# Kernel optimization log

Hardware: AMD Instinct MI355X
Metric: run time of the kernel (lower is better)

## Reference

```python
import jax, jax.numpy as jnp
import numpy as np

B, L, D = 8, 2048, 2048
NH, HD = 32, 64          # num_heads, head_dim (D = NH*HD)
CS = 16                  # inner_net_chunk_size
BASE_LR = 1.0            # inner-loop base learning rate
EPS = 1e-6
ROPE_BASE = 10000.0


def setup_inputs() -> dict:
    key = jax.random.key(0)
    ks = jax.random.split(key, 6)
    s = 0.02
    return {
        "hidden_states": jax.random.normal(ks[0], (B, L, D), jnp.float32),
        "wq": jax.random.normal(ks[1], (D, D), jnp.float32) * s,
        "wk": jax.random.normal(ks[2], (D, D), jnp.float32) * s,
        "wv": jax.random.normal(ks[3], (D, D), jnp.float32) * s,
        "wo": jax.random.normal(ks[4], (D, D), jnp.float32) * s,
        "W1": jax.random.normal(ks[5], (NH, HD, HD), jnp.float32) * s,
        "b1": jnp.zeros((NH, 1, HD), jnp.float32),
        "ttt_norm_weight": jnp.ones((NH, HD), jnp.float32),
        "ttt_norm_bias": jnp.zeros((NH, HD), jnp.float32),
    }


def _rotate_half(x):
    x1, x2 = jnp.split(x, 2, axis=-1)
    return jnp.concatenate((-x2, x1), axis=-1)


def _permute_qk(x):
    b, h, l, f = x.shape
    return x.reshape(b, h, l, f // 2, 2).transpose(0, 1, 2, 4, 3).reshape(b, h, l, f)


def _undo_permute_qk(x):
    b, h, l, f = x.shape
    return x.reshape(b, h, l, 2, f // 2).transpose(0, 1, 2, 4, 3).reshape(b, h, l, f)


def _ln_fwd(x, g, b):
    mu = x.mean(-1, keepdims=True)
    var = ((x - mu) ** 2).mean(-1, keepdims=True)
    xh = (x - mu) * jax.lax.rsqrt(var + EPS)
    return g * xh + b


def _ln_fused_l2_bwd(x, target, g, b):
    # grad of 0.5*||LN(x) - target||^2 w.r.t. x, fused (TTT inner-loop loss grad)
    f = x.shape[-1]
    mu = x.mean(-1, keepdims=True)
    var = ((x - mu) ** 2).mean(-1, keepdims=True)
    std = jnp.sqrt(var + EPS)
    xh = (x - mu) / std
    gout = (g * xh + b) - target
    gxh = gout * g
    return (f * gxh - gxh.sum(-1, keepdims=True)
            - xh * (gxh * xh).sum(-1, keepdims=True)) / (f * std)


def reference(hidden_states, wq, wk, wv, wo, W1, b1, ttt_norm_weight, ttt_norm_bias):
    Bx, Lx, Dx = hidden_states.shape
    nc = Lx // CS

    def proj(w):  # [B,L,D] -> [B,NH,L,HD]
        return (hidden_states @ w).reshape(Bx, Lx, NH, HD).transpose(0, 2, 1, 3)

    XQ, XK, XV = proj(wq), proj(wk), proj(wv)

    # rotary embedding (with permute/undo as in the source)
    inv_freq = 1.0 / (ROPE_BASE ** (jnp.arange(0, HD, 2, dtype=jnp.float32) / HD))
    freqs = jnp.outer(jnp.arange(Lx, dtype=jnp.float32), inv_freq)
    emb = jnp.concatenate((freqs, freqs), axis=-1)
    cos, sin = jnp.cos(emb)[None, None], jnp.sin(emb)[None, None]
    XQ, XK = _permute_qk(XQ), _permute_qk(XK)
    XQ = XQ * cos + _rotate_half(XQ) * sin
    XK = XK * cos + _rotate_half(XK) * sin
    XQ, XK = _undo_permute_qk(XQ), _undo_permute_qk(XK)

    def chunk(x):  # [B,NH,L,HD] -> [nc,B,NH,CS,HD]
        return x.reshape(Bx, NH, nc, CS, HD).transpose(2, 0, 1, 3, 4)

    XQc, XKc, XVc = chunk(XQ), chunk(XK), chunk(XV)

    g = ttt_norm_weight[None, :, None, :]   # [1,NH,1,HD]
    bb = ttt_norm_bias[None, :, None, :]

    token_idx = 1.0 / jnp.arange(1, CS + 1, dtype=jnp.float32)   # buffer from __init__
    eta = BASE_LR * token_idx                                    # [CS]
    tril_eta = jnp.tril(jnp.ones((CS, CS), jnp.float32)) * eta[:, None]
    last_eta = eta[-1]

    W1_0 = jnp.broadcast_to(W1[None], (Bx, NH, HD, HD))
    b1_0 = jnp.broadcast_to(b1[None], (Bx, NH, 1, HD))

    def step(carry, xs):
        W1s, b1s = carry
        xq, xk, xv = xs                                          # [B,NH,CS,HD]
        Z1 = jnp.einsum('bhkf,bhfg->bhkg', xk, W1s) + b1s
        grad = _ln_fused_l2_bwd(Z1, xv - xk, g, bb)              # dl/dZ1
        attn = jnp.tril(jnp.einsum('bhkf,bhlf->bhkl', xq, xk))   # causal within chunk
        b1_bar = b1s - jnp.einsum('kl,bhlf->bhkf', tril_eta, grad)
        Z1_bar = (jnp.einsum('bhkf,bhfg->bhkg', xq, W1s)
                  - jnp.einsum('bhkl,bhlf->bhkf', eta[None, None, :, None] * attn, grad)
                  + b1_bar)
        W1_new = W1s - last_eta * jnp.einsum('bhkf,bhkg->bhfg', xk, grad)
        b1_new = b1s - last_eta * grad.sum(-2, keepdims=True)
        out = xq + _ln_fwd(Z1_bar, g, bb)                        # residual + post-LN
        return (W1_new, b1_new), out

    _, outs = jax.lax.scan(step, (W1_0, b1_0), (XQc, XKc, XVc))  # [nc,B,NH,CS,HD]
    out = (outs.transpose(1, 2, 0, 3, 4).reshape(Bx, NH, Lx, HD)
               .transpose(0, 2, 1, 3).reshape(Bx, Lx, Dx))
    return out @ wo
```

## Files before the change

kernel.cpp:

```cpp
#include <hip/hip_runtime.h>

typedef __bf16 bf16;
typedef __bf16 bf16x4 __attribute__((ext_vector_type(4)));
typedef __bf16 bf16x8 __attribute__((ext_vector_type(8)));
typedef float floatx4 __attribute__((ext_vector_type(4)));

#define BB 8
#define LL 2048
#define DD 2048
#define NHH 32
#define HDD 64

#define MFMA16(a, b, c) __builtin_amdgcn_mfma_f32_16x16x32_bf16(a, b, c, 0, 0, 0)

__device__ __forceinline__ void gl_lds16(const void* g, void* l) {
  __builtin_amdgcn_global_load_lds((const __attribute__((address_space(1))) void*)g,
                                   (__attribute__((address_space(3))) void*)l, 16, 0, 0);
}

__global__ __launch_bounds__(256) void cast_bf16(const float* __restrict__ src,
                                                 bf16* __restrict__ dst)
{
  size_t i = ((size_t)blockIdx.x * 256 + threadIdx.x) * 8;
  floatx4 a = *(const floatx4*)(src + i);
  floatx4 b = *(const floatx4*)(src + i + 4);
  bf16x8 v;
  v[0] = (bf16)a[0]; v[1] = (bf16)a[1]; v[2] = (bf16)a[2]; v[3] = (bf16)a[3];
  v[4] = (bf16)b[0]; v[5] = (bf16)b[1]; v[6] = (bf16)b[2]; v[7] = (bf16)b[3];
  *(bf16x8*)(dst + i) = v;
}

__global__ __launch_bounds__(256) void transpose1(const float* __restrict__ src,
                                                  bf16* __restrict__ dst)
{
  __shared__ float tile[64][65];
  const int t = threadIdx.x;
  const int col = t & 63, rw = t >> 6;
  const int bx = blockIdx.x * 64, by = blockIdx.y * 64;
  for (int i = rw; i < 64; i += 4)
    tile[i][col] = src[(size_t)(by + i) * DD + bx + col];
  __syncthreads();
  for (int i = rw; i < 64; i += 4)
    dst[(size_t)(bx + i) * DD + by + col] = (bf16)tile[col][i];
}

template<int AIDX, int EPI, int RP>
__global__ __launch_bounds__(256) void gemm_bt(const bf16* __restrict__ Ab,
    const bf16* __restrict__ BT, void* __restrict__ Cv)
{
  constexpr int Kd = 2048;
  __shared__ alignas(16) bf16 As[128 * 64];
  __shared__ alignas(16) bf16 Bs[128 * 64];
  const int t = threadIdx.x;
  const int id = blockIdx.y * 16 + blockIdx.x;
  const int swz = (id & 7) * 256 + (id >> 3);
  const int bn = swz & 15, bm = swz >> 4;
  const int wave = t >> 6, lane = t & 63;
  const int m16 = lane & 15, quad = lane >> 4;
  floatx4 acc[2][8] = {};
  const int r0 = t >> 3;
  const int scc = (t & 7) ^ (r0 & 7);
  const bf16* Bb = BT + (size_t)(bn * 128) * Kd;
  char* AsB = (char*)As + wave * 1024;
  char* BsB = (char*)Bs + wave * 1024;

  for (int k0 = 0; k0 < Kd; k0 += 64) {
    for (int i = 0; i < 4; ++i) {
      int r = r0 + 32 * i;
      int col = k0 + scc * 8;
      const bf16* ga;
      if (AIDX == 0) {
        ga = Ab + (size_t)(bm * 128 + r) * Kd + col;
      } else {
        int R = bm * 128 + r;
        int b = R >> 11, l = R & 2047;
        int h = col >> 6, f = col & 63;
        ga = Ab + (((size_t)(b * NHH + h) * LL + l) * HDD + f);
      }
      gl_lds16(ga, AsB + i * 4096);
      gl_lds16(Bb + (size_t)r * Kd + col, BsB + i * 4096);
    }
    __syncthreads();
    const int sw = m16 & 7;
    for (int kk = 0; kk < 2; ++kk) {
      bf16x8 af[2], bfr[8];
      const int c = ((kk * 4 + quad) ^ sw) * 8;
      for (int mt = 0; mt < 2; ++mt)
        af[mt] = *(const bf16x8*)&As[(wave * 32 + mt * 16 + m16) * 64 + c];
      for (int nt = 0; nt < 8; ++nt)
        bfr[nt] = *(const bf16x8*)&Bs[(nt * 16 + m16) * 64 + c];
      for (int mt = 0; mt < 2; ++mt)
        for (int nt = 0; nt < 8; ++nt)
          acc[mt][nt] = MFMA16(af[mt], bfr[nt], acc[mt][nt]);
    }
    __syncthreads();
  }

  float invf[8];
  if (RP) {
#pragma unroll
    for (int nt = 0; nt < 8; ++nt) {
      int col = bn * 128 + nt * 16 + m16;
      int i = (col >> 1) & 31;
      invf[nt] = __expf(-(float)i * 0.28782313662425573f);
    }
  }

  for (int mt = 0; mt < 2; ++mt)
    for (int nt = 0; nt < 8; ++nt)
      for (int rg = 0; rg < 4; ++rg) {
        int row = bm * 128 + wave * 32 + mt * 16 + quad * 4 + rg;
        int col = bn * 128 + nt * 16 + m16;
        float v = acc[mt][nt][rg];
        if (RP) {
          float o = __shfl_xor(v, 1, 64);
          float sn, cs;
          __sincosf((float)(row & 2047) * invf[nt], &sn, &cs);
          v = (m16 & 1) ? (v * cs + o * sn) : (v * cs - o * sn);
        }
        if (EPI == 0) {
          ((float*)Cv)[(size_t)row * DD + col] = v;
        } else {
          int b = row >> 11, l = row & 2047;
          int h = col >> 6, f = col & 63;
          ((bf16*)Cv)[((size_t)(b * NHH + h) * LL + l) * HDD + f] = (bf16)v;
        }
      }
}

__global__ __launch_bounds__(256) void ttt_scan(
    const bf16* Q, const bf16* __restrict__ Kx,
    const bf16* __restrict__ V, const float* __restrict__ W1g,
    const float* __restrict__ b1g, const float* __restrict__ gw,
    const float* __restrict__ gb, bf16* O)
{
  const int bh = blockIdx.x, h = bh & 31;
  const int t = threadIdx.x;
  const int wave = t >> 6, lane = t & 63;
  const int q = lane >> 4, i16 = lane & 15;
  const int kr = t >> 4, sr = t & 15, f0 = sr * 4;

  __shared__ alignas(16) bf16 W1Th[64 * 72];
  __shared__ alignas(16) bf16 W1Tl[64 * 72];
  __shared__ alignas(16) bf16 xkTs[64 * 24];
  __shared__ alignas(16) bf16 gTh[64 * 24];
  __shared__ alignas(16) bf16 gTl[64 * 24];
  __shared__ alignas(16) bf16 Pm[16 * 24];
  __shared__ alignas(16) float Z1s[2][16 * 68];

  floatx4 accW[4];
  const float* Wg = W1g + (size_t)h * 4096;
  for (int mt = 0; mt < 4; ++mt)
    for (int r = 0; r < 4; ++r)
      accW[mt][r] = Wg[(16 * mt + 4 * q + r) * 64 + 16 * wave + i16];
  float b1r = b1g[h * 64 + 16 * wave + i16];

  for (int mt = 0; mt < 4; ++mt) {
    bf16x4 h4, l4;
    for (int r = 0; r < 4; ++r) {
      float w = accW[mt][r];
      bf16 hi = (bf16)w;
      h4[r] = hi; l4[r] = (bf16)(w - (float)hi);
    }
    int base = (16 * wave + i16) * 72 + 16 * mt + 4 * q;
    *(bf16x4*)&W1Th[base] = h4;
    *(bf16x4*)&W1Tl[base] = l4;
  }

  float gq[4], bq[4];
  for (int j = 0; j < 4; ++j) {
    gq[j] = gw[h * 64 + f0 + j];
    bq[j] = gb[h * 64 + f0 + j];
  }
  float etar[4];
  for (int r = 0; r < 4; ++r) etar[r] = 1.0f / (float)(4 * q + r + 1);

  const size_t qbase = (size_t)bh * (LL * HDD);
  const int foff = i16 * 64 + q * 8;
  const int poff = kr * 64 + f0;

  bf16x8 ak0 = *(const bf16x8*)(Kx + qbase + foff);
  bf16x8 ak1 = *(const bf16x8*)(Kx + qbase + foff + 32);
  bf16x8 aq0 = *(const bf16x8*)(Q  + qbase + foff);
  bf16x8 aq1 = *(const bf16x8*)(Q  + qbase + foff + 32);
  bf16x4 rq = *(const bf16x4*)(Q  + qbase + poff);
  bf16x4 rk = *(const bf16x4*)(Kx + qbase + poff);
  bf16x4 rv = *(const bf16x4*)(V  + qbase + poff);

  __syncthreads();

  for (int c = 0; c < 128; ++c) {
    const int pb = c & 1;
    for (int j = 0; j < 4; ++j)
      xkTs[(f0 + j) * 24 + kr] = (bf16)((float)rk[j] * -0.0625f);

    bf16x8 whi[2], wlo[2];
    {
      int wb = (16 * wave + i16) * 72 + q * 8;
      whi[0] = *(const bf16x8*)&W1Th[wb];
      whi[1] = *(const bf16x8*)&W1Th[wb + 32];
      wlo[0] = *(const bf16x8*)&W1Tl[wb];
      wlo[1] = *(const bf16x8*)&W1Tl[wb + 32];
    }
    {
      floatx4 z = {b1r, b1r, b1r, b1r};
      z = MFMA16(ak0, whi[0], z);
      z = MFMA16(ak1, whi[1], z);
      z = MFMA16(ak0, wlo[0], z);
      z = MFMA16(ak1, wlo[1], z);
      for (int r = 0; r < 4; ++r)
        Z1s[pb][(4 * q + r) * 68 + 16 * wave + i16] = z[r];
    }
    if (wave == 0) {
      floatx4 at = {};
      at = MFMA16(aq0, ak0, at);
      at = MFMA16(aq1, ak1, at);
      for (int r = 0; r < 4; ++r) {
        int krow = 4 * q + r;
        float pv = (i16 <= krow) ? -(at[r] + 1.0f) * etar[r] : 0.0f;
        Pm[krow * 24 + i16] = (bf16)pv;
      }
    }
    __syncthreads();

    {
      floatx4 z4 = *(const floatx4*)&Z1s[pb][kr * 68 + f0];
      float tg[4], sum = 0.f, ssq = 0.f;
      for (int j = 0; j < 4; ++j) {
        tg[j] = (float)rv[j] - (float)rk[j];
        sum += z4[j]; ssq += z4[j] * z4[j];
      }
      for (int m = 1; m < 16; m <<= 1) { sum += __shfl_xor(sum, m, 64); ssq += __shfl_xor(ssq, m, 64); }
      float mu = sum * (1.f / 64.f);
      float var = ssq * (1.f / 64.f) - mu * mu;
      float rstd = rsqrtf(var + 1e-6f);
      float xh[4], gx[4], s1 = 0.f, s2 = 0.f;
      for (int j = 0; j < 4; ++j) {
        xh[j] = (z4[j] - mu) * rstd;
        float go = gq[j] * xh[j] + bq[j] - tg[j];
        gx[j] = go * gq[j];
        s1 += gx[j]; s2 += gx[j] * xh[j];
      }
      for (int m = 1; m < 16; m <<= 1) { s1 += __shfl_xor(s1, m, 64); s2 += __shfl_xor(s2, m, 64); }
      for (int j = 0; j < 4; ++j) {
        float gr = (64.f * gx[j] - s1 - xh[j] * s2) * (rstd * (1.f / 64.f));
        bf16 hi = (bf16)gr;
        gTh[(f0 + j) * 24 + kr] = hi;
        gTl[(f0 + j) * 24 + kr] = (bf16)(gr - (float)hi);
      }
    }
    __syncthreads();

    const size_t nb = qbase + (size_t)(c + 1) * 1024;
    bf16x8 nak0 = *(const bf16x8*)(Kx + nb + foff);
    bf16x8 nak1 = *(const bf16x8*)(Kx + nb + foff + 32);
    bf16x8 naq0 = *(const bf16x8*)(Q  + nb + foff);
    bf16x8 naq1 = *(const bf16x8*)(Q  + nb + foff + 32);
    bf16x4 nrq = *(const bf16x4*)(Q  + nb + poff);
    bf16x4 nrk = *(const bf16x4*)(Kx + nb + poff);
    bf16x4 nrv = *(const bf16x4*)(V  + nb + poff);

    {
      bf16x8 pf  = *(const bf16x8*)&Pm[i16 * 24 + (q & 1) * 8];
      const bf16* gT = (q < 2) ? gTh : gTl;
      bf16x8 bgp = *(const bf16x8*)&gT[(16 * wave + i16) * 24 + (q & 1) * 8];
      floatx4 zb = {b1r, b1r, b1r, b1r};
      zb = MFMA16(aq0, whi[0], zb);
      zb = MFMA16(aq1, whi[1], zb);
      zb = MFMA16(aq0, wlo[0], zb);
      zb = MFMA16(aq1, wlo[1], zb);
      zb = MFMA16(pf, bgp, zb);
      for (int r = 0; r < 4; ++r)
        Z1s[pb][(4 * q + r) * 68 + 16 * wave + i16] = zb[r];

      for (int mt = 0; mt < 4; ++mt) {
        bf16x8 axk = *(const bf16x8*)&xkTs[(16 * mt + i16) * 24 + (q & 1) * 8];
        accW[mt] = MFMA16(axk, bgp, accW[mt]);
      }
      for (int mt = 0; mt < 4; ++mt) {
        bf16x4 h4, l4;
        for (int r = 0; r < 4; ++r) {
          float w = accW[mt][r];
          bf16 hi = (bf16)w;
          h4[r] = hi; l4[r] = (bf16)(w - (float)hi);
        }
        int base = (16 * wave + i16) * 72 + 16 * mt + 4 * q;
        *(bf16x4*)&W1Th[base] = h4;
        *(bf16x4*)&W1Tl[base] = l4;
      }
      {
        const bf16* rh = &gTh[(16 * wave + i16) * 24];
        const bf16* rl = &gTl[(16 * wave + i16) * 24];
        bf16x8 a0 = *(const bf16x8*)rh, a1 = *(const bf16x8*)(rh + 8);
        bf16x8 a2 = *(const bf16x8*)rl, a3 = *(const bf16x8*)(rl + 8);
        float s = 0.f;
        for (int j = 0; j < 8; ++j)
          s += (float)a0[j] + (float)a1[j] + (float)a2[j] + (float)a3[j];
        b1r -= 0.0625f * s;
      }
    }
    __syncthreads();

    {
      floatx4 z4 = *(const floatx4*)&Z1s[pb][kr * 68 + f0];
      float sum = 0.f, ssq = 0.f;
      for (int j = 0; j < 4; ++j) { sum += z4[j]; ssq += z4[j] * z4[j]; }
      for (int m = 1; m < 16; m <<= 1) { sum += __shfl_xor(sum, m, 64); ssq += __shfl_xor(ssq, m, 64); }
      float mu = sum * (1.f / 64.f);
      float var = ssq * (1.f / 64.f) - mu * mu;
      float rstd = rsqrtf(var + 1e-6f);
      bf16x4 o4;
      for (int j = 0; j < 4; ++j)
        o4[j] = (bf16)((float)rq[j] + gq[j] * ((z4[j] - mu) * rstd) + bq[j]);
      *(bf16x4*)(O + qbase + (size_t)c * 1024 + poff) = o4;
    }
    ak0 = nak0; ak1 = nak1; aq0 = naq0; aq1 = naq1;
    rq = nrq; rk = nrk; rv = nrv;
  }
}

extern "C" void kernel_launch(void* const* d_in, const int* in_sizes, int n_in,
                              void* d_out, int out_size, void* d_ws, size_t ws_size,
                              hipStream_t stream)
{
  const float* X  = (const float*)d_in[0];
  const float* wq = (const float*)d_in[1];
  const float* wk = (const float*)d_in[2];
  const float* wv = (const float*)d_in[3];
  const float* wo = (const float*)d_in[4];
  const float* W1 = (const float*)d_in[5];
  const float* b1 = (const float*)d_in[6];
  const float* gw = (const float*)d_in[7];
  const float* gb = (const float*)d_in[8];

  bf16* ws = (bf16*)d_ws;
  const size_t NEl = (size_t)BB * LL * DD;
  bf16* Qb = ws;
  bf16* Kb = ws + NEl;
  bf16* WT = ws + 2 * NEl;
  bf16* Vb = (bf16*)d_out;
  bf16* Xb = (bf16*)d_out + NEl;

  cast_bf16<<<dim3(16384), 256, 0, stream>>>(X, Xb);
  transpose1<<<dim3(32, 32), 256, 0, stream>>>(wq, WT);
  gemm_bt<0, 1, 1><<<dim3(16, 128), 256, 0, stream>>>(Xb, WT, Qb);
  transpose1<<<dim3(32, 32), 256, 0, stream>>>(wk, WT);
  gemm_bt<0, 1, 1><<<dim3(16, 128), 256, 0, stream>>>(Xb, WT, Kb);
  transpose1<<<dim3(32, 32), 256, 0, stream>>>(wv, WT);
  gemm_bt<0, 1, 0><<<dim3(16, 128), 256, 0, stream>>>(Xb, WT, Vb);
  ttt_scan<<<dim3(256), 256, 0, stream>>>(Qb, Kb, Vb, W1, b1, gw, gb, Qb);
  transpose1<<<dim3(32, 32), 256, 0, stream>>>(wo, WT);
  gemm_bt<1, 0, 0><<<dim3(16, 128), 256, 0, stream>>>(Qb, WT, d_out);
}
```

Measured before the change: 1.202 ms.

## Fuse Q, K, V projections into one GEMM sharing the X tile

Replaces three separate projection GEMMs with a single 512-thread kernel that loads each X tile once and multiplies it against all three transposed weight tiles, applying rotary embedding in the epilogue for Q and K. All three weight transposes now live in separate buffers so they can be used together. A fallback path converts fp32 X to bf16 on the fly inside the GEMM when the workspace is too small. This cuts X reads to a third and removes launches, but it raises register pressure with 24 accumulator tiles per wave and uses more shared memory per block.

```diff
diff --git a/kernel.cpp b/kernel.cpp
--- a/kernel.cpp
+++ b/kernel.cpp
@@ -42,6 +42,115 @@
   __syncthreads();
   for (int i = rw; i < 64; i += 4)
     dst[(size_t)(bx + i) * DD + by + col] = (bf16)tile[col][i];
+}
+
+template<int AFP>
+__global__ __launch_bounds__(512) void gemm_qkv(const void* __restrict__ Xv,
+    const bf16* __restrict__ BTq, const bf16* __restrict__ BTk,
+    const bf16* __restrict__ BTv,
+    bf16* __restrict__ Qo, bf16* __restrict__ Ko, bf16* __restrict__ Vo)
+{
+  constexpr int Kd = 2048;
+  __shared__ alignas(16) bf16 As[128 * 64];
+  __shared__ alignas(16) bf16 Bs[3][128 * 64];
+  const int t = threadIdx.x;
+  const int id = blockIdx.y * 16 + blockIdx.x;
+  const int swz = (id & 7) * 256 + (id >> 3);
+  const int bn = swz & 15, bm = swz >> 4;
+  const int wv = t >> 6, lane = t & 63;
+  const int q = lane >> 4, i16 = lane & 15;
+  const int wm = wv >> 2, wn = wv & 3;
+  const int srow = lane >> 3, scol = lane & 7;
+
+  floatx4 acc[3][4][2] = {};
+  char* AsB = (char*)As + wv * 2048;
+  const bf16* Bg[3] = {BTq, BTk, BTv};
+
+  for (int k0 = 0; k0 < Kd; k0 += 64) {
+#pragma unroll
+    for (int i = 0; i < 2; ++i) {
+      int r = (wv * 2 + i) * 8 + srow;
+      int cc = scol ^ (r & 7);
+      if (AFP == 0) {
+        gl_lds16((const bf16*)Xv + (size_t)(bm * 128 + r) * Kd + k0 + cc * 8,
+                 AsB + i * 1024);
+      } else {
+        const float* src = (const float*)Xv + (size_t)(bm * 128 + r) * Kd + k0 + cc * 8;
+        floatx4 f0 = *(const floatx4*)src;
+        floatx4 f1 = *(const floatx4*)(src + 4);
+        bf16x8 v;
+        v[0] = (bf16)f0[0]; v[1] = (bf16)f0[1]; v[2] = (bf16)f0[2]; v[3] = (bf16)f0[3];
+        v[4] = (bf16)f1[0]; v[5] = (bf16)f1[1]; v[6] = (bf16)f1[2]; v[7] = (bf16)f1[3];
+        *(bf16x8*)((char*)As + (wv * 2 + i) * 1024 + lane * 16) = v;
+      }
+    }
+#pragma unroll
+    for (int w = 0; w < 3; ++w)
+#pragma unroll
+      for (int i = 0; i < 2; ++i) {
+        int r = (wv * 2 + i) * 8 + srow;
+        int cc = scol ^ (r & 7);
+        gl_lds16(Bg[w] + (size_t)(bn * 128 + r) * Kd + k0 + cc * 8,
+                 (char*)Bs[w] + wv * 2048 + i * 1024);
+      }
+    __syncthreads();
+
+#pragma unroll
+    for (int kk = 0; kk < 2; ++kk) {
+      bf16x8 af[4];
+#pragma unroll
+      for (int mt = 0; mt < 4; ++mt) {
+        int r = wm * 64 + mt * 16 + i16;
+        af[mt] = *(const bf16x8*)&As[r * 64 + ((kk * 4 + q) ^ (r & 7)) * 8];
+      }
+#pragma unroll
+      for (int w = 0; w < 3; ++w) {
+        bf16x8 bfr[2];
+#pragma unroll
+        for (int nt = 0; nt < 2; ++nt) {
+          int r = wn * 32 + nt * 16 + i16;
+          bfr[nt] = *(const bf16x8*)&Bs[w][r * 64 + ((kk * 4 + q) ^ (r & 7)) * 8];
+        }
+#pragma unroll
+        for (int mt = 0; mt < 4; ++mt)
+#pragma unroll
+          for (int nt = 0; nt < 2; ++nt)
+            acc[w][mt][nt] = MFMA16(af[mt], bfr[nt], acc[w][mt][nt]);
+      }
+    }
+    __syncthreads();
+  }
+
+  float invf[2];
+#pragma unroll
+  for (int nt = 0; nt < 2; ++nt) {
+    int col = bn * 128 + wn * 32 + nt * 16 + i16;
+    int i = (col >> 1) & 31;
+    invf[nt] = __expf(-(float)i * 0.28782313662425573f);
+  }
+#pragma unroll
+  for (int w = 0; w < 3; ++w) {
+    bf16* Co = (w == 0) ? Qo : (w == 1) ? Ko : Vo;
+#pragma unroll
+    for (int mt = 0; mt < 4; ++mt)
+#pragma unroll
+      for (int nt = 0; nt < 2; ++nt)
+#pragma unroll
+        for (int rg = 0; rg < 4; ++rg) {
+          int row = bm * 128 + wm * 64 + mt * 16 + q * 4 + rg;
+          int col = bn * 128 + wn * 32 + nt * 16 + i16;
+          float v = acc[w][mt][nt][rg];
+          if (w < 2) {
+            float o = __shfl_xor(v, 1, 64);
+            float sn, cs;
+            __sincosf((float)(row & 2047) * invf[nt], &sn, &cs);
+            v = (i16 & 1) ? (v * cs + o * sn) : (v * cs - o * sn);
+          }
+          int b = row >> 11, l = row & 2047;
+          int h = col >> 6, f = col & 63;
+          Co[((size_t)(b * NHH + h) * LL + l) * HDD + f] = (bf16)v;
+        }
+  }
 }
 
 template<int AIDX, int EPI, int RP>
@@ -335,20 +444,36 @@
 
   bf16* ws = (bf16*)d_ws;
   const size_t NEl = (size_t)BB * LL * DD;
+  const size_t WEl = (size_t)DD * DD;
   bf16* Qb = ws;
   bf16* Kb = ws + NEl;
-  bf16* WT = ws + 2 * NEl;
   bf16* Vb = (bf16*)d_out;
-  bf16* Xb = (bf16*)d_out + NEl;
-
-  cast_bf16<<<dim3(16384), 256, 0, stream>>>(X, Xb);
-  transpose1<<<dim3(32, 32), 256, 0, stream>>>(wq, WT);
-  gemm_bt<0, 1, 1><<<dim3(16, 128), 256, 0, stream>>>(Xb, WT, Qb);
-  transpose1<<<dim3(32, 32), 256, 0, stream>>>(wk, WT);
-  gemm_bt<0, 1, 1><<<dim3(16, 128), 256, 0, stream>>>(Xb, WT, Kb);
-  transpose1<<<dim3(32, 32), 256, 0, stream>>>(wv, WT);
-  gemm_bt<0, 1, 0><<<dim3(16, 128), 256, 0, stream>>>(Xb, WT, Vb);
-  ttt_scan<<<dim3(256), 256, 0, stream>>>(Qb, Kb, Vb, W1, b1, gw, gb, Qb);
-  transpose1<<<dim3(32, 32), 256, 0, stream>>>(wo, WT);
-  gemm_bt<1, 0, 0><<<dim3(16, 128), 256, 0, stream>>>(Qb, WT, d_out);
-}
+
+  const size_t need = (2 * NEl + 3 * WEl) * sizeof(bf16);
+  if (ws_size >= need) {
+    bf16* BTq = ws + 2 * NEl;
+    bf16* BTk = BTq + WEl;
+    bf16* BTv = BTk + WEl;
+    bf16* Xb  = (bf16*)d_out + NEl;
+    cast_bf16<<<dim3(16384), 256, 0, stream>>>(X, Xb);
+    transpose1<<<dim3(32, 32), 256, 0, stream>>>(wq, BTq);
+    transpose1<<<dim3(32, 32), 256, 0, stream>>>(wk, BTk);
+    transpose1<<<dim3(32, 32), 256, 0, stream>>>(wv, BTv);
+    gemm_qkv<0><<<dim3(16, 128), 512, 0, stream>>>(Xb, BTq, BTk, BTv, Qb, Kb, Vb);
+    ttt_scan<<<dim3(256), 256, 0, stream>>>(Qb, Kb, Vb, W1, b1, gw, gb, Qb);
+    transpose1<<<dim3(32, 32), 256, 0, stream>>>(wo, BTq);
+    gemm_bt<1, 0, 0><<<dim3(16, 128), 256, 0, stream>>>(Qb, BTq, d_out);
+  } else {
+    bf16* BTq = (bf16*)d_out + NEl;
+    bf16* BTk = BTq + WEl;
+    bf16* BTv = BTk + WEl;
+    bf16* WT  = ws + 2 * NEl;
+    transpose1<<<dim3(32, 32), 256, 0, stream>>>(wq, BTq);
+    transpose1<<<dim3(32, 32), 256, 0, stream>>>(wk, BTk);
+    transpose1<<<dim3(32, 32), 256, 0, stream>>>(wv, BTv);
+    gemm_qkv<1><<<dim3(16, 128), 512, 0, stream>>>(X, BTq, BTk, BTv, Qb, Kb, Vb);
+    ttt_scan<<<dim3(256), 256, 0, stream>>>(Qb, Kb, Vb, W1, b1, gw, gb, Qb);
+    transpose1<<<dim3(32, 32), 256, 0, stream>>>(wo, WT);
+    gemm_bt<1, 0, 0><<<dim3(16, 128), 256, 0, stream>>>(Qb, WT, d_out);
+  }
+}
```

Result: slower. 1.329 ms (+10.5%).

## Replace GEMM with 256x256-tile, 512-thread kernel using 4-stage LDS pipeline

Applied to the files above, without the earlier changes.

Swaps the 128x128 single-buffered bf16 GEMM for a 256x256 tile kernel with 8 waves, a K-step of 32 and a 4-slot shared-memory ring fed by async global-to-LDS loads issued three stages ahead. The goal is to hide global memory latency behind MFMA work and raise arithmetic intensity per block, using raised wave priority around the MFMA block. The costs are 128KB of LDS per block, a large accumulator register footprint per thread, and fewer blocks in flight, which may reduce occupancy. The last loop iterations issue wrapped-around extra loads that are never consumed.

```diff
diff --git a/kernel.cpp b/kernel.cpp
--- a/kernel.cpp
+++ b/kernel.cpp
@@ -45,78 +45,100 @@
 }
 
 template<int AIDX, int EPI, int RP>
-__global__ __launch_bounds__(256) void gemm_bt(const bf16* __restrict__ Ab,
+__global__ __launch_bounds__(512) void gemm256(const bf16* __restrict__ Ab,
     const bf16* __restrict__ BT, void* __restrict__ Cv)
 {
-  constexpr int Kd = 2048;
-  __shared__ alignas(16) bf16 As[128 * 64];
-  __shared__ alignas(16) bf16 Bs[128 * 64];
+  constexpr int NT = 64;
+  __shared__ alignas(16) bf16 P[4][2][8192];
   const int t = threadIdx.x;
-  const int id = blockIdx.y * 16 + blockIdx.x;
-  const int swz = (id & 7) * 256 + (id >> 3);
-  const int bn = swz & 15, bm = swz >> 4;
-  const int wave = t >> 6, lane = t & 63;
-  const int m16 = lane & 15, quad = lane >> 4;
-  floatx4 acc[2][8] = {};
-  const int r0 = t >> 3;
-  const int scc = (t & 7) ^ (r0 & 7);
-  const bf16* Bb = BT + (size_t)(bn * 128) * Kd;
-  char* AsB = (char*)As + wave * 1024;
-  char* BsB = (char*)Bs + wave * 1024;
-
-  for (int k0 = 0; k0 < Kd; k0 += 64) {
-    for (int i = 0; i < 4; ++i) {
-      int r = r0 + 32 * i;
-      int col = k0 + scc * 8;
+  const int id = blockIdx.y * 8 + blockIdx.x;
+  const int swz = (id & 7) * 64 + (id >> 3);
+  const int bm = swz >> 3, bn = swz & 7;
+  const int wv = t >> 6, lane = t & 63;
+  const int q = lane >> 4, i16 = lane & 15;
+  const int wm = wv >> 2, wn = wv & 3;
+
+  floatx4 acc[8][4] = {};
+
+  const int cswz = ((lane & 3) ^ ((lane >> 2) & 3)) * 8;
+  int srow[2];
+  srow[0] = wv * 16 + (lane >> 2);
+  srow[1] = 128 + wv * 16 + (lane >> 2);
+  size_t aSrc[2], bSrc[2];
+#pragma unroll
+  for (int j = 0; j < 2; ++j) {
+    int rA = bm * 256 + srow[j];
+    if (AIDX == 0) {
+      aSrc[j] = (size_t)rA * DD + cswz;
+    } else {
+      int b = rA >> 11, l = rA & 2047;
+      aSrc[j] = ((size_t)b * NHH * LL + l) * HDD + cswz;
+    }
+    bSrc[j] = (size_t)(bn * 256 + srow[j]) * DD + cswz;
+  }
+
+  auto STAGE = [&](int st) {
+    const int slot = st & 3;
+#pragma unroll
+    for (int j = 0; j < 2; ++j) {
       const bf16* ga;
-      if (AIDX == 0) {
-        ga = Ab + (size_t)(bm * 128 + r) * Kd + col;
-      } else {
-        int R = bm * 128 + r;
-        int b = R >> 11, l = R & 2047;
-        int h = col >> 6, f = col & 63;
-        ga = Ab + (((size_t)(b * NHH + h) * LL + l) * HDD + f);
-      }
-      gl_lds16(ga, AsB + i * 4096);
-      gl_lds16(Bb + (size_t)r * Kd + col, BsB + i * 4096);
-    }
-    __syncthreads();
-    const int sw = m16 & 7;
-    for (int kk = 0; kk < 2; ++kk) {
-      bf16x8 af[2], bfr[8];
-      const int c = ((kk * 4 + quad) ^ sw) * 8;
-      for (int mt = 0; mt < 2; ++mt)
-        af[mt] = *(const bf16x8*)&As[(wave * 32 + mt * 16 + m16) * 64 + c];
-      for (int nt = 0; nt < 8; ++nt)
-        bfr[nt] = *(const bf16x8*)&Bs[(nt * 16 + m16) * 64 + c];
-      for (int mt = 0; mt < 2; ++mt)
-        for (int nt = 0; nt < 8; ++nt)
-          acc[mt][nt] = MFMA16(af[mt], bfr[nt], acc[mt][nt]);
-    }
-    __syncthreads();
-  }
-
-  float invf[8];
+      if (AIDX == 0) ga = Ab + aSrc[j] + st * 32;
+      else           ga = Ab + aSrc[j] + (size_t)(st >> 1) * (LL * HDD) + (st & 1) * 32;
+      gl_lds16(ga, &P[slot][0][(j * 8 + wv) * 512]);
+      gl_lds16(BT + bSrc[j] + st * 32, &P[slot][1][(j * 8 + wv) * 512]);
+    }
+  };
+
+  STAGE(0); STAGE(1); STAGE(2);
+
+  for (int st = 0; st < NT; ++st) {
+    asm volatile("s_waitcnt vmcnt(8)\n\ts_barrier" ::: "memory");
+    STAGE((st + 3) & (NT - 1));
+    const bf16* Ap = &P[st & 3][0][0];
+    const bf16* Bp = &P[st & 3][1][0];
+    bf16x8 af[8], bfr[4];
+#pragma unroll
+    for (int nt = 0; nt < 4; ++nt) {
+      int r = wn * 64 + nt * 16 + i16;
+      bfr[nt] = *(const bf16x8*)&Bp[r * 32 + ((q ^ (r & 3)) << 3)];
+    }
+#pragma unroll
+    for (int mt = 0; mt < 8; ++mt) {
+      int r = wm * 128 + mt * 16 + i16;
+      af[mt] = *(const bf16x8*)&Ap[r * 32 + ((q ^ (r & 3)) << 3)];
+    }
+    __builtin_amdgcn_s_setprio(1);
+#pragma unroll
+    for (int mt = 0; mt < 8; ++mt)
+#pragma unroll
+      for (int nt = 0; nt < 4; ++nt)
+        acc[mt][nt] = MFMA16(af[mt], bfr[nt], acc[mt][nt]);
+    __builtin_amdgcn_s_setprio(0);
+    asm volatile("s_waitcnt lgkmcnt(0)" ::: "memory");
+  }
+
+  float invf[4];
   if (RP) {
 #pragma unroll
-    for (int nt = 0; nt < 8; ++nt) {
-      int col = bn * 128 + nt * 16 + m16;
-      int i = (col >> 1) & 31;
-      invf[nt] = __expf(-(float)i * 0.28782313662425573f);
-    }
-  }
-
-  for (int mt = 0; mt < 2; ++mt)
-    for (int nt = 0; nt < 8; ++nt)
+    for (int nt = 0; nt < 4; ++nt) {
+      int col = bn * 256 + wn * 64 + nt * 16 + i16;
+      invf[nt] = __expf(-(float)((col >> 1) & 31) * 0.28782313662425573f);
+    }
+  }
+#pragma unroll
+  for (int mt = 0; mt < 8; ++mt)
+#pragma unroll
+    for (int nt = 0; nt < 4; ++nt)
+#pragma unroll
       for (int rg = 0; rg < 4; ++rg) {
-        int row = bm * 128 + wave * 32 + mt * 16 + quad * 4 + rg;
-        int col = bn * 128 + nt * 16 + m16;
+        int row = bm * 256 + wm * 128 + mt * 16 + q * 4 + rg;
+        int col = bn * 256 + wn * 64 + nt * 16 + i16;
         float v = acc[mt][nt][rg];
         if (RP) {
           float o = __shfl_xor(v, 1, 64);
           float sn, cs;
           __sincosf((float)(row & 2047) * invf[nt], &sn, &cs);
-          v = (m16 & 1) ? (v * cs + o * sn) : (v * cs - o * sn);
+          v = (i16 & 1) ? (v * cs + o * sn) : (v * cs - o * sn);
         }
         if (EPI == 0) {
           ((float*)Cv)[(size_t)row * DD + col] = v;
@@ -343,12 +365,12 @@
 
   cast_bf16<<<dim3(16384), 256, 0, stream>>>(X, Xb);
   transpose1<<<dim3(32, 32), 256, 0, stream>>>(wq, WT);
-  gemm_bt<0, 1, 1><<<dim3(16, 128), 256, 0, stream>>>(Xb, WT, Qb);
+  gemm256<0, 1, 1><<<dim3(8, 64), 512, 0, stream>>>(Xb, WT, Qb);
   transpose1<<<dim3(32, 32), 256, 0, stream>>>(wk, WT);
-  gemm_bt<0, 1, 1><<<dim3(16, 128), 256, 0, stream>>>(Xb, WT, Kb);
+  gemm256<0, 1, 1><<<dim3(8, 64), 512, 0, stream>>>(Xb, WT, Kb);
   transpose1<<<dim3(32, 32), 256, 0, stream>>>(wv, WT);
-  gemm_bt<0, 1, 0><<<dim3(16, 128), 256, 0, stream>>>(Xb, WT, Vb);
+  gemm256<0, 1, 0><<<dim3(8, 64), 512, 0, stream>>>(Xb, WT, Vb);
   ttt_scan<<<dim3(256), 256, 0, stream>>>(Qb, Kb, Vb, W1, b1, gw, gb, Qb);
   transpose1<<<dim3(32, 32), 256, 0, stream>>>(wo, WT);
-  gemm_bt<1, 0, 0><<<dim3(16, 128), 256, 0, stream>>>(Qb, WT, d_out);
-}
+  gemm256<1, 0, 0><<<dim3(8, 64), 512, 0, stream>>>(Qb, WT, d_out);
+}
```

Result: faster. 1.074 ms (-10.6%).
